# Kernel tuning notes

Measured on AMD Instinct MI355X. Metric: run time of the kernel, lower is better.

The kernel has to match this reference:

```python
import jax, jax.numpy as jnp
import numpy as np

B, L, D, CH, H = 16384, 50, 20, 16, 6


def setup_inputs() -> dict:
    key = jax.random.key(0)
    ks = jax.random.split(key, 18)
    s = 0.1
    return {
        "x": jax.random.normal(ks[0], (B, L, D), jnp.float32),
        "we_w": jax.random.normal(ks[1], (CH, D), jnp.float32) * s,
        "we_b": jax.random.normal(ks[2], (CH,), jnp.float32) * s,
        "attn_w": jax.random.normal(ks[3], (CH, CH), jnp.float32) * s,
        "attn_b": jax.random.normal(ks[4], (CH,), jnp.float32) * s,
        "conv1_w": jax.random.normal(ks[5], (CH, CH, 1), jnp.float32) * s,
        "conv1_b": jax.random.normal(ks[6], (CH,), jnp.float32) * s,
        "conv2_w": jax.random.normal(ks[7], (CH, CH, 3), jnp.float32) * s,
        "conv2_b": jax.random.normal(ks[8], (CH,), jnp.float32) * s,
        "conv3_w": jax.random.normal(ks[9], (CH, CH, 5), jnp.float32) * s,
        "conv3_b": jax.random.normal(ks[10], (CH,), jnp.float32) * s,
        "gru_wih": jax.random.normal(ks[11], (3 * H, CH), jnp.float32) * s,
        "gru_whh": jax.random.normal(ks[12], (3 * H, H), jnp.float32) * s,
        "gru_bih": jax.random.normal(ks[13], (3 * H,), jnp.float32) * s,
        "gru_bhh": jax.random.normal(ks[14], (3 * H,), jnp.float32) * s,
        "fc3_w": jax.random.normal(ks[15], (2, 3 * CH + H), jnp.float32) * s,
        "fc3_b": jax.random.normal(ks[16], (2,), jnp.float32) * s,
        "batchsize": B,
    }


def _conv1d(x, w, b, pad):
    # x: [B, C, L], w: [O, I, K] -> [B, O, L]
    y = jax.lax.conv_general_dilated(x, w, (1,), [(pad, pad)],
                                     dimension_numbers=("NCH", "OIH", "NCH"))
    return y + b[None, :, None]


def _gru(xg, wih, whh, bih, bhh):
    # xg: [B, L, CH] -> outputs [B, L, H] (PyTorch GRU equations, h0=0)
    gi = jnp.einsum("blc,gc->blg", xg, wih) + bih  # [B, L, 3H]
    gi_t = jnp.swapaxes(gi, 0, 1)                  # [L, B, 3H]
    h0 = jnp.zeros((xg.shape[0], H), xg.dtype)

    def step(h, gi_step):
        gh = h @ whh.T + bhh
        i_r, i_z, i_n = jnp.split(gi_step, 3, axis=-1)
        h_r, h_z, h_n = jnp.split(gh, 3, axis=-1)
        r = jax.nn.sigmoid(i_r + h_r)
        z = jax.nn.sigmoid(i_z + h_z)
        n = jnp.tanh(i_n + r * h_n)
        h_new = (1.0 - z) * n + z * h
        return h_new, h_new

    _, outs = jax.lax.scan(step, h0, gi_t)
    return jnp.swapaxes(outs, 0, 1)  # [B, L, H]


def reference(x, we_w, we_b, attn_w, attn_b, conv1_w, conv1_b, conv2_w, conv2_b,
              conv3_w, conv3_b, gru_wih, gru_whh, gru_bih, gru_bhh, fc3_w, fc3_b,
              batchsize):
    b = batchsize
    xe = x @ we_w.T + we_b                 # [B, L, CH]
    xr = xe.reshape(b, CH, L)              # RESHAPE (not transpose), as in torch

    lrelu = lambda v: jnp.where(v > 0, v, 0.1 * v)
    x1 = lrelu(_conv1d(xr, conv1_w, conv1_b, 0))
    x2 = lrelu(_conv1d(xr, conv2_w, conv2_b, 1))
    x3 = lrelu(_conv1d(xr, conv3_w, conv3_b, 2))

    xg = xr.reshape(b, L, CH)              # == xe
    x4 = _gru(xg, gru_wih, gru_whh, gru_bih, gru_bhh)  # [B, L, H]

    # dotproduct1: note x4.reshape([B,H,L]) is a reshape, NOT a transpose
    scores = jnp.matmul(x4, x4.reshape(b, H, L)) / H   # [B, L, L]
    alphas = jax.nn.softmax(scores, axis=1)            # softmax over dim=1 as in torch
    y = jnp.matmul(alphas, x4).reshape(b, H, L)        # [B, H, L]
    x_gru = jnp.sum(y, axis=2)                         # [B, H]

    # vectorized per-timestep attention loop: x[:, :, i] over i -> swapaxes
    xt = jnp.swapaxes(xr, 1, 2)                        # [B, L, CH]
    attn = jnp.tanh(xt @ attn_w.T + attn_b)            # [B, L, CH]
    attn1 = jnp.concatenate([attn, attn, attn], axis=2).reshape(b, 3 * CH, L)

    x_cat = jnp.concatenate([x1, x2, x3], axis=1)      # [B, 3CH, L]
    x_cnn = jnp.sum(x_cat * attn1, axis=2)             # [B, 3CH]

    feat = jnp.concatenate([x_cnn, x_gru], axis=1)     # [B, 3CH+H]
    return feat @ fc3_w.T + fc3_b                      # [B, 2]
```

## Files before the change

kernel.cpp:

```cpp
#include <hip/hip_runtime.h>

#define BATCH 16384
#define LSEQ  50
#define DIN   20
#define CHN   16
#define HID   6

typedef float vf2 __attribute__((ext_vector_type(2)));

__device__ __forceinline__ float frcp(float x){ return __builtin_amdgcn_rcpf(x); }
__device__ __forceinline__ float fexp2(float x){
#if __has_builtin(__builtin_amdgcn_exp2f)
  return __builtin_amdgcn_exp2f(x);
#else
  return exp2f(x);
#endif
}
#define LOG2E 1.4426950408889634f
__device__ __forceinline__ float fsig(float x){ return frcp(1.0f + fexp2(-LOG2E * x)); }
__device__ __forceinline__ float ftanh(float x){ float t = fexp2((2.0f*LOG2E)*x); return (t - 1.0f) * frcp(t + 1.0f); }
__device__ __forceinline__ float lrelu(float v){ return v > 0.0f ? v : 0.1f*v; }
__device__ __forceinline__ vf2 fma2(vf2 a, vf2 b, vf2 c){
#if __has_builtin(__builtin_elementwise_fma)
  return __builtin_elementwise_fma(a, b, c);
#else
  vf2 r; r.x = fmaf(a.x, b.x, c.x); r.y = fmaf(a.y, b.y, c.y); return r;
#endif
}
#define KEXP 0.24044917348149793f

#define WAVE_FENCE() asm volatile("s_waitcnt lgkmcnt(0)" ::: "memory")

constexpr int SLAB = 2040;

__global__ __launch_bounds__(128, 4) void fused_kernel(
    const float* __restrict__ x,
    const float* __restrict__ we_w, const float* __restrict__ we_b,
    const float* __restrict__ attn_w, const float* __restrict__ attn_b,
    const float* __restrict__ c1w, const float* __restrict__ c1b,
    const float* __restrict__ c2w, const float* __restrict__ c2b,
    const float* __restrict__ c3w, const float* __restrict__ c3b,
    const float* __restrict__ wih, const float* __restrict__ whh,
    const float* __restrict__ bih, const float* __restrict__ bhh,
    const float* __restrict__ fc3w, const float* __restrict__ fc3b,
    float* __restrict__ out)
{
  __shared__ __align__(16) float smem[2 * SLAB];
  const int tid  = threadIdx.x;
  const int wave = tid >> 6;
  const int lane = tid & 63;
  const int b    = blockIdx.x * 2 + wave;

  float* S    = smem + wave * SLAB;
  float* sXEp = S;
  float* sY   = S;
  float* R1   = S + 840;
  float* sFE  = S + 1672;
  float* sX4  = S + 1740;

  const float* xb = x + (size_t)b * (LSEQ * DIN);

  if (lane < CHN) {
    sXEp[lane * 52]     = 0.0f;
    sXEp[lane * 52 + 1] = 0.0f;
  } else if (lane == 16) {
    sXEp[832] = 0.0f;
    sXEp[833] = 0.0f;
  }

  if (lane < LSEQ) {
    vf2 xv2[10];
    const float4* xr = (const float4*)(xb + lane * DIN);
    #pragma unroll
    for (int q = 0; q < 5; ++q) {
      float4 v = xr[q];
      vf2 p0; p0.x = v.x; p0.y = v.y;
      vf2 p1; p1.x = v.z; p1.y = v.w;
      xv2[2*q] = p0; xv2[2*q+1] = p1;
    }
    float xe[CHN];
    #pragma unroll
    for (int c = 0; c < CHN; ++c) {
      const vf2* wr = (const vf2*)(we_w + c * DIN);
      vf2 a2; a2.x = we_b[c]; a2.y = 0.0f;
      #pragma unroll
      for (int dp = 0; dp < 10; ++dp) a2 = fma2(xv2[dp], wr[dp], a2);
      xe[c] = a2.x + a2.y;
    }
    const int kk0 = lane * CHN;
    const int i0  = kk0 / 50;
    const int m0  = kk0 - i0 * 50;
    float* basep = sXEp + i0 * 52 + 2 + m0;
    #pragma unroll
    for (int c = 0; c < CHN; ++c) {
      const int off = c + ((m0 + c >= 50) ? 2 : 0);
      basep[off] = xe[c];
    }
    vf2 xe2[8];
    #pragma unroll
    for (int p = 0; p < 8; ++p) { xe2[p].x = xe[2*p]; xe2[p].y = xe[2*p+1]; }
    float gi[18];
    #pragma unroll
    for (int g = 0; g < 18; ++g) {
      const vf2* wr = (const vf2*)(wih + g * CHN);
      vf2 a2; a2.x = bih[g]; a2.y = 0.0f;
      #pragma unroll
      for (int p = 0; p < 8; ++p) a2 = fma2(xe2[p], wr[p], a2);
      gi[g] = a2.x + a2.y;
    }
    float2* gd = (float2*)(R1 + lane * 18);
    #pragma unroll
    for (int p = 0; p < 9; ++p) gd[p] = make_float2(gi[2*p], gi[2*p+1]);
  }
  WAVE_FENCE();

  if (lane < 16) {
    const int g  = lane;
    const int gb = 16 + (g & 1);
    vf2 wa2[3], wb2[3];
    #pragma unroll
    for (int k = 0; k < 3; ++k) {
      const float2 a = *(const float2*)(whh + g  * HID + 2*k);
      const float2 c = *(const float2*)(whh + gb * HID + 2*k);
      wa2[k].x = a.x; wa2[k].y = a.y;
      wb2[k].x = c.x; wb2[k].y = c.y;
    }
    const float ba = bhh[g];
    const float bb = bhh[gb];
    const int srcZ = 6 + g;
    const int srcN = (g < 4) ? (12 + g) : (g - 4);

    vf2 hh2[3];
    #pragma unroll
    for (int k = 0; k < 3; ++k) hh2[k] = (vf2)0.0f;
    float hprev = 0.0f;

    const float* gp = R1;
    for (int l = 0; l < LSEQ; ++l) {
      const float gia = gp[g];
      const float gib = gp[gb];
      gp += 18;
      vf2 aa; aa.x = ba; aa.y = 0.0f;
      vf2 ab; ab.x = bb; ab.y = 0.0f;
      #pragma unroll
      for (int k = 0; k < 3; ++k) {
        aa = fma2(wa2[k], hh2[k], aa);
        ab = fma2(wb2[k], hh2[k], ab);
      }
      const float gha = aa.x + aa.y;
      const float ghb = ab.x + ab.y;
      const float siga = fsig(gia + gha);
      const float ghx = (g >= 12) ? gha : ghb;
      const float gix = (g >= 12) ? gia : gib;
      const float ghn = __shfl(ghx, srcN);
      const float gin = __shfl(gix, srcN);
      const float z   = __shfl(siga, srcZ);
      const float n   = ftanh(fmaf(siga, ghn, gin));
      const float hn  = fmaf(z, hprev - n, n);
      hprev = hn;
      if (g < HID) sX4[l * HID + g] = hn;
      const float2 h01 = *(const float2*)(sX4 + l * HID);
      const float2 h23 = *(const float2*)(sX4 + l * HID + 2);
      const float2 h45 = *(const float2*)(sX4 + l * HID + 4);
      hh2[0].x = h01.x; hh2[0].y = h01.y;
      hh2[1].x = h23.x; hh2[1].y = h23.y;
      hh2[2].x = h45.x; hh2[2].y = h45.y;
    }
  }
  WAVE_FENCE();

  {
    float* sATt = R1;
    if (lane < LSEQ) {
      float a[CHN];
      #pragma unroll
      for (int cc = 0; cc < CHN; ++cc) a[cc] = sXEp[cc * 52 + 2 + lane];
      vf2 a2[8];
      #pragma unroll
      for (int p = 0; p < 8; ++p) { a2[p].x = a[2*p]; a2[p].y = a[2*p+1]; }
      #pragma unroll
      for (int c = 0; c < CHN; ++c) {
        const vf2* wr = (const vf2*)(attn_w + c * CHN);
        vf2 s2; s2.x = attn_b[c]; s2.y = 0.0f;
        #pragma unroll
        for (int p = 0; p < 8; ++p) s2 = fma2(a2[p], wr[p], s2);
        sATt[c * 52 + lane] = ftanh(s2.x + s2.y);
      }
    }
  }
  WAVE_FENCE();

  {
    const float* sATt = R1;
    const int o   = lane & 15;
    const int seg = lane >> 4;
    const int s   = seg * 12;
    const int NL  = (seg == 3) ? 14 : 12;
    vf2 Z1[7], Z2[7], Z3[7];
    #pragma unroll
    for (int p = 0; p < 7; ++p) {
      Z1[p] = (vf2)0.0f; Z2[p] = (vf2)0.0f; Z3[p] = (vf2)0.0f;
    }
    for (int i = 0; i < CHN; ++i) {
      const float w1s = c1w[o * CHN + i];
      vf2 W1; W1.x = w1s; W1.y = w1s;
      vf2 W2[3], W3[5];
      #pragma unroll
      for (int t = 0; t < 3; ++t) { float w = c2w[(o * CHN + i) * 3 + t]; W2[t].x = w; W2[t].y = w; }
      #pragma unroll
      for (int t = 0; t < 5; ++t) { float w = c3w[(o * CHN + i) * 5 + t]; W3[t].x = w; W3[t].y = w; }
      const float4* wp = (const float4*)(sXEp + i * 52 + s);
      float4 q0 = wp[0], q1 = wp[1], q2 = wp[2], q3 = wp[3], q4 = wp[4];
      float xv[20] = {q0.x,q0.y,q0.z,q0.w, q1.x,q1.y,q1.z,q1.w,
                      q2.x,q2.y,q2.z,q2.w, q3.x,q3.y,q3.z,q3.w,
                      q4.x,q4.y,q4.z,q4.w};
      vf2 XP[17];
      #pragma unroll
      for (int a = 0; a < 17; ++a) { XP[a].x = xv[a]; XP[a].y = xv[a+1]; }
      #pragma unroll
      for (int p = 0; p < 7; ++p) {
        Z1[p] = fma2(W1, XP[2*p + 2], Z1[p]);
        Z2[p] = fma2(W2[0], XP[2*p + 1], Z2[p]);
        Z2[p] = fma2(W2[1], XP[2*p + 2], Z2[p]);
        Z2[p] = fma2(W2[2], XP[2*p + 3], Z2[p]);
        Z3[p] = fma2(W3[0], XP[2*p    ], Z3[p]);
        Z3[p] = fma2(W3[1], XP[2*p + 1], Z3[p]);
        Z3[p] = fma2(W3[2], XP[2*p + 2], Z3[p]);
        Z3[p] = fma2(W3[3], XP[2*p + 3], Z3[p]);
        Z3[p] = fma2(W3[4], XP[2*p + 4], Z3[p]);
      }
    }
    const float b1v = c1b[o], b2v = c2b[o], b3v = c3b[o];
    float a1 = 0.0f, a2 = 0.0f, a3 = 0.0f;
    #pragma unroll
    for (int u = 0; u < 14; ++u) {
      if (u < NL) {
        const int l = s + u;
        const int t = 2 * o + l;
        const int col = t & 15;
        const int r1 = o + ((t >= 48) ? 1 : 0);
        const int r2 = 16 + o + ((t >= 16) ? 1 : 0) + ((t >= 64) ? 1 : 0);
        const int r3 = 33 + o + ((t >= 32) ? 1 : 0);
        float v1 = lrelu(Z1[u >> 1][u & 1] + b1v);
        float v2 = lrelu(Z2[u >> 1][u & 1] + b2v);
        float v3 = lrelu(Z3[u >> 1][u & 1] + b3v);
        a1 += v1 * sATt[col * 52 + r1];
        a2 += v2 * sATt[col * 52 + r2];
        a3 += v3 * sATt[col * 52 + r3];
      }
    }
    a1 += __shfl_xor(a1, 16); a1 += __shfl_xor(a1, 32);
    a2 += __shfl_xor(a2, 16); a2 += __shfl_xor(a2, 32);
    a3 += __shfl_xor(a3, 16); a3 += __shfl_xor(a3, 32);
    if (lane < CHN) { sFE[o] = a1; sFE[CHN + o] = a2; sFE[2 * CHN + o] = a3; }
  }
  WAVE_FENCE();

  float* sC = R1;
  vf2 ri2[3];
  if (lane < LSEQ) {
    const int xw = ((lane >> 1) & 3) << 2;
    float* rp = sC + lane * 16;
    float colj[HID];
    #pragma unroll
    for (int h = 0; h < HID; ++h) colj[h] = sX4[h * LSEQ + lane];
    vf2 cj2[3];
    #pragma unroll
    for (int p = 0; p < 3; ++p) { cj2[p].x = colj[2*p]; cj2[p].y = colj[2*p+1]; }
    *(float4*)(rp + xw)       = make_float4(colj[0], colj[1], colj[2], colj[3]);
    *(float2*)(rp + (4 ^ xw)) = make_float2(colj[4], colj[5]);
    float zs0 = 0.0f, zs1 = 0.0f;
    #pragma unroll
    for (int i = 0; i < LSEQ; i += 2) {
      const float2 r0 = *(const float2*)(sX4 + i * 6);
      const float2 r1 = *(const float2*)(sX4 + i * 6 + 2);
      const float2 r2 = *(const float2*)(sX4 + i * 6 + 4);
      vf2 s2 = (vf2)0.0f;
      vf2 p0; p0.x = r0.x; p0.y = r0.y;
      vf2 p1; p1.x = r1.x; p1.y = r1.y;
      vf2 p2; p2.x = r2.x; p2.y = r2.y;
      s2 = fma2(p0, cj2[0], s2);
      s2 = fma2(p1, cj2[1], s2);
      s2 = fma2(p2, cj2[2], s2);
      zs0 += fexp2((s2.x + s2.y) * KEXP);
      const float2 t0 = *(const float2*)(sX4 + (i + 1) * 6);
      const float2 t1 = *(const float2*)(sX4 + (i + 1) * 6 + 2);
      const float2 t2 = *(const float2*)(sX4 + (i + 1) * 6 + 4);
      vf2 u2 = (vf2)0.0f;
      vf2 v0; v0.x = t0.x; v0.y = t0.y;
      vf2 v1; v1.x = t1.x; v1.y = t1.y;
      vf2 v2; v2.x = t2.x; v2.y = t2.y;
      u2 = fma2(v0, cj2[0], u2);
      u2 = fma2(v1, cj2[1], u2);
      u2 = fma2(v2, cj2[2], u2);
      zs1 += fexp2((u2.x + u2.y) * KEXP);
    }
    const float zi = frcp(zs0 + zs1);
    const float2 q0 = *(const float2*)(sX4 + lane * 6);
    const float2 q1 = *(const float2*)(sX4 + lane * 6 + 2);
    const float2 q2 = *(const float2*)(sX4 + lane * 6 + 4);
    ri2[0].x = q0.x; ri2[0].y = q0.y;
    ri2[1].x = q1.x; ri2[1].y = q1.y;
    ri2[2].x = q2.x; ri2[2].y = q2.y;
    *(float4*)(rp + (8 ^ xw))  = make_float4(zi*q0.x, zi*q0.y, zi*q1.x, zi*q1.y);
    *(float2*)(rp + (12 ^ xw)) = make_float2(zi*q2.x, zi*q2.y);
  }
  WAVE_FENCE();

  if (lane < LSEQ) {
    vf2 ya2[3];
    #pragma unroll
    for (int p = 0; p < 3; ++p) ya2[p] = (vf2)0.0f;
    auto acc_row = [&](const float* rp, const int xw) {
      const float4 t0 = *(const float4*)(rp + xw);
      const float2 t1 = *(const float2*)(rp + (4 ^ xw));
      vf2 p0; p0.x = t0.x; p0.y = t0.y;
      vf2 p1; p1.x = t0.z; p1.y = t0.w;
      vf2 p2; p2.x = t1.x; p2.y = t1.y;
      vf2 s2 = (vf2)0.0f;
      s2 = fma2(ri2[0], p0, s2);
      s2 = fma2(ri2[1], p1, s2);
      s2 = fma2(ri2[2], p2, s2);
      const float e = fexp2((s2.x + s2.y) * KEXP);
      vf2 e2; e2.x = e; e2.y = e;
      const float4 w0 = *(const float4*)(rp + (8 ^ xw));
      const float2 w1 = *(const float2*)(rp + (12 ^ xw));
      vf2 wv0; wv0.x = w0.x; wv0.y = w0.y;
      vf2 wv1; wv1.x = w0.z; wv1.y = w0.w;
      vf2 wv2; wv2.x = w1.x; wv2.y = w1.y;
      ya2[0] = fma2(e2, wv0, ya2[0]);
      ya2[1] = fma2(e2, wv1, ya2[1]);
      ya2[2] = fma2(e2, wv2, ya2[2]);
    };
    for (int jb = 0; jb < 48; jb += 8) {
      const float* cp = sC + jb * 16;
      #pragma unroll
      for (int d = 0; d < 8; ++d) acc_row(cp + d * 16, ((d >> 1) & 3) << 2);
    }
    acc_row(sC + 48 * 16, 0);
    acc_row(sC + 49 * 16, 0);
    *(float2*)(sY + lane * 6)     = make_float2(ya2[0].x, ya2[0].y);
    *(float2*)(sY + lane * 6 + 2) = make_float2(ya2[1].x, ya2[1].y);
    *(float2*)(sY + lane * 6 + 4) = make_float2(ya2[2].x, ya2[2].y);
  }
  WAVE_FENCE();

  if (lane < 48) {
    const int h = lane >> 3;
    const int m = lane & 7;
    float s = 0.0f;
    #pragma unroll
    for (int k = 0; k < 7; ++k) {
      const int idx = m + (k << 3);
      if (idx < LSEQ) s += sY[h * LSEQ + idx];
    }
    s += __shfl_xor(s, 1);
    s += __shfl_xor(s, 2);
    s += __shfl_xor(s, 4);
    if (m == 0) sFE[48 + h] = s;
  }
  WAVE_FENCE();

  {
    const int oo = lane & 1;
    const int kk = lane >> 1;
    float s = fc3w[oo * 54 + kk] * sFE[kk];
    if (kk < 22) s = fmaf(fc3w[oo * 54 + kk + 32], sFE[kk + 32], s);
    s += __shfl_xor(s, 2);
    s += __shfl_xor(s, 4);
    s += __shfl_xor(s, 8);
    s += __shfl_xor(s, 16);
    s += __shfl_xor(s, 32);
    if (lane < 2) out[(size_t)b * 2 + lane] = s + fc3b[lane];
  }
}

extern "C" void kernel_launch(void* const* d_in, const int* in_sizes, int n_in,
                              void* d_out, int out_size, void* d_ws, size_t ws_size,
                              hipStream_t stream) {
  (void)in_sizes; (void)n_in; (void)d_ws; (void)ws_size; (void)out_size;
  fused_kernel<<<BATCH / 2, 128, 0, stream>>>(
      (const float*)d_in[0],
      (const float*)d_in[1],  (const float*)d_in[2],
      (const float*)d_in[3],  (const float*)d_in[4],
      (const float*)d_in[5],  (const float*)d_in[6],
      (const float*)d_in[7],  (const float*)d_in[8],
      (const float*)d_in[9],  (const float*)d_in[10],
      (const float*)d_in[11], (const float*)d_in[12],
      (const float*)d_in[13], (const float*)d_in[14],
      (const float*)d_in[15], (const float*)d_in[16],
      (float*)d_out);
}
```

Baseline: 276.2 us.

## Use one-wave blocks and per-hidden-unit GRU lanes with prefetched gates

Switches from two waves per 128-thread block to one wave per 64-thread block, with one batch element per block and its own shared slab. The GRU recurrence is rewritten so six lanes each compute the r, z and n gates for one hidden unit. This removes the cross-lane shuffles from the serial step, and the gate inputs are stored interleaved so the next step's values can be prefetched. The conv epilogue also drops the per-iteration predicate and instead handles the two extra timesteps only for the last segment. The costs are twice as many blocks to launch and schedule, and a somewhat longer per-lane dependency chain in each GRU step.

```diff
diff --git a/kernel.cpp b/kernel.cpp
--- a/kernel.cpp
+++ b/kernel.cpp
@@ -33,7 +33,7 @@
 
 constexpr int SLAB = 2040;
 
-__global__ __launch_bounds__(128, 4) void fused_kernel(
+__global__ __launch_bounds__(64, 4) void fused_kernel(
     const float* __restrict__ x,
     const float* __restrict__ we_w, const float* __restrict__ we_b,
     const float* __restrict__ attn_w, const float* __restrict__ attn_b,
@@ -45,13 +45,11 @@
     const float* __restrict__ fc3w, const float* __restrict__ fc3b,
     float* __restrict__ out)
 {
-  __shared__ __align__(16) float smem[2 * SLAB];
-  const int tid  = threadIdx.x;
-  const int wave = tid >> 6;
-  const int lane = tid & 63;
-  const int b    = blockIdx.x * 2 + wave;
-
-  float* S    = smem + wave * SLAB;
+  __shared__ __align__(16) float smem[SLAB];
+  const int lane = threadIdx.x;
+  const int b    = blockIdx.x;
+
+  float* S    = smem;
   float* sXEp = S;
   float* sY   = S;
   float* R1   = S + 840;
@@ -109,56 +107,65 @@
       gi[g] = a2.x + a2.y;
     }
     float2* gd = (float2*)(R1 + lane * 18);
-    #pragma unroll
-    for (int p = 0; p < 9; ++p) gd[p] = make_float2(gi[2*p], gi[2*p+1]);
-  }
-  WAVE_FENCE();
-
-  if (lane < 16) {
-    const int g  = lane;
-    const int gb = 16 + (g & 1);
-    vf2 wa2[3], wb2[3];
+    gd[0] = make_float2(gi[0],  gi[6]);
+    gd[1] = make_float2(gi[12], gi[1]);
+    gd[2] = make_float2(gi[7],  gi[13]);
+    gd[3] = make_float2(gi[2],  gi[8]);
+    gd[4] = make_float2(gi[14], gi[3]);
+    gd[5] = make_float2(gi[9],  gi[15]);
+    gd[6] = make_float2(gi[4],  gi[10]);
+    gd[7] = make_float2(gi[16], gi[5]);
+    gd[8] = make_float2(gi[11], gi[17]);
+  }
+  WAVE_FENCE();
+
+  if (lane < HID) {
+    const int h = lane;
+    vf2 wr2[3], wz2[3], wn2[3];
     #pragma unroll
     for (int k = 0; k < 3; ++k) {
-      const float2 a = *(const float2*)(whh + g  * HID + 2*k);
-      const float2 c = *(const float2*)(whh + gb * HID + 2*k);
-      wa2[k].x = a.x; wa2[k].y = a.y;
-      wb2[k].x = c.x; wb2[k].y = c.y;
-    }
-    const float ba = bhh[g];
-    const float bb = bhh[gb];
-    const int srcZ = 6 + g;
-    const int srcN = (g < 4) ? (12 + g) : (g - 4);
+      const float2 a = *(const float2*)(whh + h        * HID + 2*k);
+      const float2 c = *(const float2*)(whh + (6 + h)  * HID + 2*k);
+      const float2 d = *(const float2*)(whh + (12 + h) * HID + 2*k);
+      wr2[k].x = a.x; wr2[k].y = a.y;
+      wz2[k].x = c.x; wz2[k].y = c.y;
+      wn2[k].x = d.x; wn2[k].y = d.y;
+    }
+    const float br = bhh[h], bz = bhh[6 + h], bn = bhh[12 + h];
 
     vf2 hh2[3];
     #pragma unroll
     for (int k = 0; k < 3; ++k) hh2[k] = (vf2)0.0f;
     float hprev = 0.0f;
 
-    const float* gp = R1;
+    const float* gp = R1 + 3 * h;
+    float gR = gp[0];
+    float gZ = gp[1];
+    float gN = gp[2];
     for (int l = 0; l < LSEQ; ++l) {
-      const float gia = gp[g];
-      const float gib = gp[gb];
+      const float gir = gR, giz = gZ, gin = gN;
       gp += 18;
-      vf2 aa; aa.x = ba; aa.y = 0.0f;
-      vf2 ab; ab.x = bb; ab.y = 0.0f;
+      gR = gp[0];
+      gZ = gp[1];
+      gN = gp[2];
+      vf2 ar; ar.x = br; ar.y = 0.0f;
+      vf2 az; az.x = bz; az.y = 0.0f;
+      vf2 an; an.x = bn; an.y = 0.0f;
       #pragma unroll
       for (int k = 0; k < 3; ++k) {
-        aa = fma2(wa2[k], hh2[k], aa);
-        ab = fma2(wb2[k], hh2[k], ab);
+        ar = fma2(wr2[k], hh2[k], ar);
+        az = fma2(wz2[k], hh2[k], az);
+        an = fma2(wn2[k], hh2[k], an);
       }
-      const float gha = aa.x + aa.y;
-      const float ghb = ab.x + ab.y;
-      const float siga = fsig(gia + gha);
-      const float ghx = (g >= 12) ? gha : ghb;
-      const float gix = (g >= 12) ? gia : gib;
-      const float ghn = __shfl(ghx, srcN);
-      const float gin = __shfl(gix, srcN);
-      const float z   = __shfl(siga, srcZ);
-      const float n   = ftanh(fmaf(siga, ghn, gin));
-      const float hn  = fmaf(z, hprev - n, n);
+      const float dr = ar.x + ar.y;
+      const float dz = az.x + az.y;
+      const float dn = an.x + an.y;
+      const float r  = fsig(gir + dr);
+      const float z  = fsig(giz + dz);
+      const float n  = ftanh(fmaf(r, dn, gin));
+      const float hn = fmaf(z, hprev - n, n);
       hprev = hn;
-      if (g < HID) sX4[l * HID + g] = hn;
+      sX4[l * HID + h] = hn;
       const float2 h01 = *(const float2*)(sX4 + l * HID);
       const float2 h23 = *(const float2*)(sX4 + l * HID + 2);
       const float2 h45 = *(const float2*)(sX4 + l * HID + 4);
@@ -195,7 +202,6 @@
     const int o   = lane & 15;
     const int seg = lane >> 4;
     const int s   = seg * 12;
-    const int NL  = (seg == 3) ? 14 : 12;
     vf2 Z1[7], Z2[7], Z3[7];
     #pragma unroll
     for (int p = 0; p < 7; ++p) {
@@ -232,23 +238,23 @@
     }
     const float b1v = c1b[o], b2v = c2b[o], b3v = c3b[o];
     float a1 = 0.0f, a2 = 0.0f, a3 = 0.0f;
-    #pragma unroll
-    for (int u = 0; u < 14; ++u) {
-      if (u < NL) {
-        const int l = s + u;
-        const int t = 2 * o + l;
-        const int col = t & 15;
-        const int r1 = o + ((t >= 48) ? 1 : 0);
-        const int r2 = 16 + o + ((t >= 16) ? 1 : 0) + ((t >= 64) ? 1 : 0);
-        const int r3 = 33 + o + ((t >= 32) ? 1 : 0);
-        float v1 = lrelu(Z1[u >> 1][u & 1] + b1v);
-        float v2 = lrelu(Z2[u >> 1][u & 1] + b2v);
-        float v3 = lrelu(Z3[u >> 1][u & 1] + b3v);
-        a1 += v1 * sATt[col * 52 + r1];
-        a2 += v2 * sATt[col * 52 + r2];
-        a3 += v3 * sATt[col * 52 + r3];
-      }
-    }
+    auto body = [&](const int u) {
+      const int l = s + u;
+      const int t = 2 * o + l;
+      const int col = t & 15;
+      const int r1 = o + ((t >= 48) ? 1 : 0);
+      const int r2 = 16 + o + ((t >= 16) ? 1 : 0) + ((t >= 64) ? 1 : 0);
+      const int r3 = 33 + o + ((t >= 32) ? 1 : 0);
+      float v1 = lrelu(Z1[u >> 1][u & 1] + b1v);
+      float v2 = lrelu(Z2[u >> 1][u & 1] + b2v);
+      float v3 = lrelu(Z3[u >> 1][u & 1] + b3v);
+      a1 += v1 * sATt[col * 52 + r1];
+      a2 += v2 * sATt[col * 52 + r2];
+      a3 += v3 * sATt[col * 52 + r3];
+    };
+    #pragma unroll
+    for (int u = 0; u < 12; ++u) body(u);
+    if (seg == 3) { body(12); body(13); }
     a1 += __shfl_xor(a1, 16); a1 += __shfl_xor(a1, 32);
     a2 += __shfl_xor(a2, 16); a2 += __shfl_xor(a2, 32);
     a3 += __shfl_xor(a3, 16); a3 += __shfl_xor(a3, 32);
@@ -379,7 +385,7 @@
                               void* d_out, int out_size, void* d_ws, size_t ws_size,
                               hipStream_t stream) {
   (void)in_sizes; (void)n_in; (void)d_ws; (void)ws_size; (void)out_size;
-  fused_kernel<<<BATCH / 2, 128, 0, stream>>>(
+  fused_kernel<<<BATCH, 64, 0, stream>>>(
       (const float*)d_in[0],
       (const float*)d_in[1],  (const float*)d_in[2],
       (const float*)d_in[3],  (const float*)d_in[4],
```

New measurement: 274.6 us (median of 2 runs). No clear change (-0.6%).
